# Optimization experiments

Hardware: AMD Instinct MI355X
Metric: run time of the kernel (lower is better)

## Reference

```python
import jax, jax.numpy as jnp
import numpy as np

BATCH = 64
N_NODES = 1000
SEQ = 12
FEAT = 4          # in_features_per_node // N_history
IN_CH = 48        # in_features_per_node, also GAT out_channels
HEADS = 2
OUT_FEAT = 2      # out_features_per_node
H1, H2 = 256, 128
N_TOTAL = BATCH * N_NODES
E = 1024000


def setup_inputs() -> dict:
    key = jax.random.key(0)
    ks = jax.random.split(key, 16)
    s = 0.05
    return {
        "x": jax.random.normal(ks[0], (N_TOTAL, IN_CH), jnp.float32),
        "edge_index": jax.random.randint(ks[1], (2, E), 0, N_TOTAL, jnp.int64),
        "W_gat": jax.random.normal(ks[2], (IN_CH, HEADS * IN_CH), jnp.float32) * s,
        "att_src": jax.random.normal(ks[3], (HEADS, IN_CH), jnp.float32) * s,
        "att_dst": jax.random.normal(ks[4], (HEADS, IN_CH), jnp.float32) * s,
        "gat_bias": jax.random.normal(ks[5], (IN_CH,), jnp.float32) * s,
        "W_ih1": jax.random.normal(ks[6], (4 * H1, N_NODES * FEAT), jnp.float32) * s,
        "W_hh1": jax.random.normal(ks[7], (4 * H1, H1), jnp.float32) * s,
        "b1": jnp.zeros((4 * H1,), jnp.float32),
        "W_ih2": jax.random.normal(ks[8], (4 * H2, H1), jnp.float32) * s,
        "W_hh2": jax.random.normal(ks[9], (4 * H2, H2), jnp.float32) * s,
        "b2": jnp.zeros((4 * H2,), jnp.float32),
        "W_out": jax.random.normal(ks[10], (N_NODES * OUT_FEAT, H2), jnp.float32) * s,
        "b_out": jnp.zeros((N_NODES * OUT_FEAT,), jnp.float32),
    }


def _gat_conv(x, edge_index, W_gat, att_src, att_dst, gat_bias):
    """PyG GATConv, heads=HEADS, concat=False (mean over heads), add_self_loops=True."""
    N = x.shape[0]
    h = (x @ W_gat).reshape(N, HEADS, IN_CH)              # [N,H,C]
    a_src = jnp.einsum('nhc,hc->nh', h, att_src)          # [N,H]
    a_dst = jnp.einsum('nhc,hc->nh', h, att_dst)
    loops = jnp.arange(N, dtype=edge_index.dtype)
    src = jnp.concatenate([edge_index[0], loops])         # [E+N]
    dst = jnp.concatenate([edge_index[1], loops])
    e = jax.nn.leaky_relu(a_src[src] + a_dst[dst], 0.2)   # [E+N,H]
    # segment-softmax over incoming edges of each destination node
    m = jnp.full((N, HEADS), -jnp.inf, e.dtype).at[dst].max(e)
    w = jnp.exp(e - m[dst])
    denom = jax.ops.segment_sum(w, dst, num_segments=N)
    alpha = w / (denom[dst] + 1e-16)                      # [E+N,H]
    msg = h[src] * alpha[:, :, None]                      # [E+N,H,C]
    out = jax.ops.segment_sum(msg, dst, num_segments=N)   # [N,H,C]
    return out.mean(axis=1) + gat_bias                    # [N,C]


def _lstm(x_seq, W_ih, W_hh, b):
    """Single-layer LSTM, PyTorch gate order (i,f,g,o). x_seq: [T,B,D]."""
    Hs = W_hh.shape[1]
    B = x_seq.shape[1]
    xw = jnp.einsum('tbd,gd->tbg', x_seq, W_ih) + b       # precompute input proj

    def step(carry, xt):
        h, c = carry
        g = xt + h @ W_hh.T
        i, f, gg, o = jnp.split(g, 4, axis=-1)
        i, f, o = jax.nn.sigmoid(i), jax.nn.sigmoid(f), jax.nn.sigmoid(o)
        c = f * c + i * jnp.tanh(gg)
        h = o * jnp.tanh(c)
        return (h, c), h

    h0 = jnp.zeros((B, Hs), x_seq.dtype)
    _, ys = jax.lax.scan(step, (h0, h0), xw)
    return ys                                             # [T,B,Hs]


def reference(x, edge_index, W_gat, att_src, att_dst, gat_bias,
              W_ih1, W_hh1, b1, W_ih2, W_hh2, b2, W_out, b_out):
    g = _gat_conv(x, edge_index, W_gat, att_src, att_dst, gat_bias)  # [N_total, 48]
    # (B, N_nodes, SEQ, FEAT) -> movedim(2,0) -> (SEQ, B, N_nodes*FEAT)
    g = g.reshape(BATCH, N_NODES, SEQ, FEAT)
    g = jnp.moveaxis(g, 2, 0).reshape(SEQ, BATCH, N_NODES * FEAT)
    y = _lstm(g, W_ih1, W_hh1, b1)
    y = _lstm(y, W_ih2, W_hh2, b2)
    last = y[-1]                                          # [B, H2]
    out = last @ W_out.T + b_out                          # [B, N_nodes*OUT_FEAT]
    return out.reshape(BATCH * N_NODES, OUT_FEAT)
```

## Files before the change

kernel.cpp:

```cpp
#include <hip/hip_runtime.h>
#include <hip/hip_fp16.h>
#include <math.h>

#define NTOT   64000
#define NNODE  1000
#define NBATCH 64
#define NSEQ   12
#define NE     1024000

typedef _Float16 half8 __attribute__((ext_vector_type(8)));
typedef float f32x4 __attribute__((ext_vector_type(4)));

__device__ __forceinline__ float lrelu(float x){ return x > 0.f ? x : 0.2f*x; }
__device__ __forceinline__ float sigmoidf_(float x){ return 1.f/(1.f+__expf(-x)); }

__global__ void __launch_bounds__(256) k_gat_count(const float* __restrict__ x, const float* __restrict__ Wg,
                       const float* __restrict__ att_s, const float* __restrict__ att_d,
                       __half* __restrict__ hfeat, float* __restrict__ asrc, float* __restrict__ adst,
                       const int* __restrict__ ei, int* __restrict__ cnt,
                       const float* __restrict__ Wih1, const float* __restrict__ Whh1,
                       const float* __restrict__ Wih2, const float* __restrict__ Whh2,
                       _Float16* __restrict__ Bh, __half* __restrict__ Wt){
  if (blockIdx.x >= 4250){
    int blk = blockIdx.x - 4250;
    if (blk < 4000){
      int i = blk*256 + threadIdx.x;
      float4 v = *(const float4*)(Wih1 + (size_t)i*4);
      union { _Float16 h[4]; uint2 u; } o;
      o.h[0] = (_Float16)v.x; o.h[1] = (_Float16)v.y;
      o.h[2] = (_Float16)v.z; o.h[3] = (_Float16)v.w;
      *(uint2*)(Bh + (size_t)i*4) = o.u;
      return;
    }
    int i = (blk-4000)*256 + threadIdx.x;
    if (i < 262144){ int q = i>>10, r = i&1023; Wt[i] = __float2half(Whh1[r*256+q]); return; }
    i -= 262144;
    if (i < 131072){ int q = i>>9, r = i&511; Wt[262144+i] = __float2half(Wih2[r*256+q]); return; }
    i -= 131072;
    if (i < 65536){ int q = i>>9, r = i&511; Wt[393216+i] = __float2half(Whh2[(size_t)r*128+q]); }
    return;
  }
  if (blockIdx.x >= 250){
    int e = (blockIdx.x - 250)*256 + threadIdx.x;
    if (e < NE) atomicAdd(&cnt[ei[NE + e]], 1);
    return;
  }
  __shared__ __align__(16) float Ws[48*96];
  __shared__ __align__(16) float as_s[96];
  __shared__ __align__(16) float ad_s[96];
  for (int i = threadIdx.x; i < 48*96; i += 256) Ws[i] = Wg[i];
  if (threadIdx.x < 96){ as_s[threadIdx.x] = att_s[threadIdx.x]; ad_s[threadIdx.x] = att_d[threadIdx.x]; }
  __syncthreads();
  int n = blockIdx.x * 256 + threadIdx.x;
  float xr[48];
  const float4* xv = (const float4*)(x + (size_t)n*48);
  #pragma unroll
  for (int q = 0; q < 12; ++q){ float4 v = xv[q]; xr[q*4]=v.x; xr[q*4+1]=v.y; xr[q*4+2]=v.z; xr[q*4+3]=v.w; }
  float a0=0.f,a1=0.f,d0=0.f,d1=0.f;
  __half* hrow = hfeat + (size_t)n*96;
  for (int j4 = 0; j4 < 96; j4 += 4){
    float ax=0.f, ay=0.f, az=0.f, aw=0.f;
    #pragma unroll 8
    for (int k = 0; k < 48; ++k){
      float4 wv = *(const float4*)&Ws[k*96 + j4];
      float xk = xr[k];
      ax += wv.x*xk; ay += wv.y*xk; az += wv.z*xk; aw += wv.w*xk;
    }
    __half2 p0; p0.x = __float2half(ax); p0.y = __float2half(ay);
    __half2 p1; p1.x = __float2half(az); p1.y = __float2half(aw);
    *(__half2*)(hrow + j4)     = p0;
    *(__half2*)(hrow + j4 + 2) = p1;
    float4 as4 = *(const float4*)&as_s[j4];
    float4 ad4 = *(const float4*)&ad_s[j4];
    float sdot = ax*as4.x + ay*as4.y + az*as4.z + aw*as4.w;
    float ddot = ax*ad4.x + ay*ad4.y + az*ad4.z + aw*ad4.w;
    if (j4 < 48){ a0 += sdot; d0 += ddot; }
    else        { a1 += sdot; d1 += ddot; }
  }
  asrc[n*2]=a0; asrc[n*2+1]=a1; adst[n*2]=d0; adst[n*2+1]=d1;
}

__global__ void __launch_bounds__(256) k_scan1(const int* __restrict__ cnt, int* __restrict__ wsum){
  int w = (blockIdx.x*256 + threadIdx.x) >> 6;
  int lane = threadIdx.x & 63;
  int v = cnt[w*64 + lane];
  int t = v;
  #pragma unroll
  for (int d = 1; d < 64; d <<= 1) t += __shfl_xor(t, d);
  if (lane == 0) wsum[w] = t;
}

__global__ void __launch_bounds__(1024) k_scan2(int* __restrict__ wsum){
  __shared__ int tmp[1024];
  int k = threadIdx.x;
  int v = (k < 1000) ? wsum[k] : 0;
  tmp[k] = v; __syncthreads();
  for (int d = 1; d < 1024; d <<= 1){
    int t = (k >= d) ? tmp[k-d] : 0;
    __syncthreads();
    tmp[k] += t;
    __syncthreads();
  }
  if (k < 1000) wsum[k] = tmp[k] - v;
}

__global__ void __launch_bounds__(256) k_scan3(const int* __restrict__ cnt, const int* __restrict__ wpre,
                                               int* __restrict__ offs, int* __restrict__ cursor){
  int w = (blockIdx.x*256 + threadIdx.x) >> 6;
  int lane = threadIdx.x & 63;
  int i = w*64 + lane;
  int v = cnt[i];
  int x = v;
  #pragma unroll
  for (int d = 1; d < 64; d <<= 1){
    int t = __shfl_up(x, d);
    if (lane >= d) x += t;
  }
  int excl = wpre[w] + x - v;
  offs[i] = excl; cursor[i] = excl;
  if (i == NTOT-1) offs[NTOT] = excl + v;
}

__global__ void k_scatter(const int* __restrict__ ei, int* __restrict__ cursor, int* __restrict__ csr){
  int e = blockIdx.x*256 + threadIdx.x;
  if (e < NE){
    int d = ei[NE + e], s = ei[e];
    int pos = atomicAdd(&cursor[d], 1);
    csr[pos] = s;
  }
}

__global__ void __launch_bounds__(256) k_node(const __half* __restrict__ hf, const float* __restrict__ asrc,
                      const float* __restrict__ adst, const int* __restrict__ offs,
                      const int* __restrict__ csr, const float* __restrict__ bias,
                      _Float16* __restrict__ xseqh){
  __shared__ float gsh[4][96];
  int wv = threadIdx.x >> 6, lane = threadIdx.x & 63;
  int n = blockIdx.x*4 + wv;
  int off = offs[n], deg = offs[n+1] - off;
  const float2* as2 = (const float2*)asrc;
  float2 adn = ((const float2*)adst)[n];
  float2 asn = as2[n];
  float es0 = __expf(lrelu(asn.x + adn.x));
  float es1 = __expf(lrelu(asn.y + adn.y));
  if (lane < 48){
    int cl = lane;
    bool h0 = (lane < 24);
    float wself = h0 ? es0 : es1;
    float ssum = wself;
    float2 acc;
    {
      __half2 r2 = *(const __half2*)(hf + (size_t)n*96 + 2*cl);
      float2 r = __half22float2(r2);
      acc.x = r.x*wself; acc.y = r.y*wself;
    }
    int i = 0;
    for (; i + 8 <= deg; i += 8){
      int ss[8];
      #pragma unroll
      for (int j = 0; j < 8; ++j) ss[j] = csr[off+i+j];
      float2 aa[8];
      #pragma unroll
      for (int j = 0; j < 8; ++j) aa[j] = as2[ss[j]];
      __half2 rr[8];
      #pragma unroll
      for (int j = 0; j < 8; ++j) rr[j] = *(const __half2*)(hf + (size_t)ss[j]*96 + 2*cl);
      #pragma unroll
      for (int j = 0; j < 8; ++j){
        float w0 = __expf(lrelu(aa[j].x + adn.x));
        float w1 = __expf(lrelu(aa[j].y + adn.y));
        float ws = h0 ? w0 : w1;
        float2 r = __half22float2(rr[j]);
        acc.x += r.x*ws; acc.y += r.y*ws;
        ssum += ws;
      }
    }
    for (; i + 4 <= deg; i += 4){
      int ss[4];
      #pragma unroll
      for (int j = 0; j < 4; ++j) ss[j] = csr[off+i+j];
      float2 aa[4];
      #pragma unroll
      for (int j = 0; j < 4; ++j) aa[j] = as2[ss[j]];
      __half2 rr[4];
      #pragma unroll
      for (int j = 0; j < 4; ++j) rr[j] = *(const __half2*)(hf + (size_t)ss[j]*96 + 2*cl);
      #pragma unroll
      for (int j = 0; j < 4; ++j){
        float w0 = __expf(lrelu(aa[j].x + adn.x));
        float w1 = __expf(lrelu(aa[j].y + adn.y));
        float ws = h0 ? w0 : w1;
        float2 r = __half22float2(rr[j]);
        acc.x += r.x*ws; acc.y += r.y*ws;
        ssum += ws;
      }
    }
    for (; i < deg; ++i){
      int s = csr[off+i];
      float2 a = as2[s];
      __half2 r2 = *(const __half2*)(hf + (size_t)s*96 + 2*cl);
      float w0 = __expf(lrelu(a.x + adn.x));
      float w1 = __expf(lrelu(a.y + adn.y));
      float ws = h0 ? w0 : w1;
      float2 r = __half22float2(r2);
      acc.x += r.x*ws; acc.y += r.y*ws;
      ssum += ws;
    }
    float inv = 1.f/(ssum + 1e-16f);
    gsh[wv][2*cl] = acc.x*inv; gsh[wv][2*cl+1] = acc.y*inv;
  }
  __syncthreads();
  if (lane < 48){
    float g = 0.5f*(gsh[wv][lane] + gsh[wv][48+lane]) + bias[lane];
    int b = n / 1000, node = n - b*1000;
    int t = lane >> 2, f = lane & 3;
    xseqh[((size_t)(t*64 + b))*4000 + node*4 + f] = (_Float16)g;
  }
}

__global__ void __launch_bounds__(256) k_gemm1h(const _Float16* __restrict__ A,
                        const _Float16* __restrict__ B, float* __restrict__ part){
  __shared__ _Float16 As[64*40];
  __shared__ _Float16 Bs[64*40];
  int tid = threadIdx.x;
  int w = tid >> 6, l = tid & 63;
  int m0 = blockIdx.x*64, n0 = blockIdx.y*64;
  int k0 = blockIdx.z*800;
  int fr = l & 15, fk = (l >> 4)*8;
  f32x4 acc0 = {0.f,0.f,0.f,0.f}, acc1 = acc0, acc2 = acc0, acc3 = acc0;
  int ra = tid >> 2, ca = (tid & 3)*8;
  const _Float16* Ap = A + (size_t)(m0+ra)*4000 + k0 + ca;
  const _Float16* Bp = B + (size_t)(n0+ra)*4000 + k0 + ca;
  _Float16* Asw = &As[ra*40 + ca];
  _Float16* Bsw = &Bs[ra*40 + ca];
  half8 pa = *(const half8*)Ap;
  half8 pb = *(const half8*)Bp;
  for (int kk = 0; kk < 800; kk += 32){
    *(half8*)Asw = pa;
    *(half8*)Bsw = pb;
    __syncthreads();
    if (kk + 32 < 800){
      pa = *(const half8*)(Ap + kk + 32);
      pb = *(const half8*)(Bp + kk + 32);
    }
    half8 af  = *(const half8*)&As[(w*16 + fr)*40 + fk];
    half8 bf0 = *(const half8*)&Bs[( 0 + fr)*40 + fk];
    half8 bf1 = *(const half8*)&Bs[(16 + fr)*40 + fk];
    half8 bf2 = *(const half8*)&Bs[(32 + fr)*40 + fk];
    half8 bf3 = *(const half8*)&Bs[(48 + fr)*40 + fk];
    acc0 = __builtin_amdgcn_mfma_f32_16x16x32_f16(af, bf0, acc0, 0, 0, 0);
    acc1 = __builtin_amdgcn_mfma_f32_16x16x32_f16(af, bf1, acc1, 0, 0, 0);
    acc2 = __builtin_amdgcn_mfma_f32_16x16x32_f16(af, bf2, acc2, 0, 0, 0);
    acc3 = __builtin_amdgcn_mfma_f32_16x16x32_f16(af, bf3, acc3, 0, 0, 0);
    __syncthreads();
  }
  int mrow = m0 + w*16 + (l >> 4)*4;
  int ncol = n0 + (l & 15);
  #pragma unroll
  for (int r = 0; r < 4; ++r){
    float* cp = part + ((size_t)blockIdx.z*768 + mrow + r)*1024 + ncol;
    cp[0]  = acc0[r];
    cp[16] = acc1[r];
    cp[32] = acc2[r];
    cp[48] = acc3[r];
  }
}

__device__ __forceinline__ void mac8(float* acc, uint4 wv, float hq){
  const __half2* hp = (const __half2*)&wv;
  float2 f0 = __half22float2(hp[0]);
  float2 f1 = __half22float2(hp[1]);
  float2 f2 = __half22float2(hp[2]);
  float2 f3 = __half22float2(hp[3]);
  acc[0] += f0.x*hq; acc[1] += f0.y*hq;
  acc[2] += f1.x*hq; acc[3] += f1.y*hq;
  acc[4] += f2.x*hq; acc[5] += f2.y*hq;
  acc[6] += f3.x*hq; acc[7] += f3.y*hq;
}

__global__ void __launch_bounds__(1024) k_lstm(
    const float* __restrict__ part, const float* __restrict__ b1,
    const __half* __restrict__ W1, const __half* __restrict__ W2i,
    const __half* __restrict__ W2h, const float* __restrict__ b2,
    float* __restrict__ h2o){
  __shared__ float h1s[256];
  __shared__ float h2s[128];
  __shared__ __align__(16) float pA[8192];
  __shared__ __align__(16) float pB[8192];
  int t = threadIdx.x;
  int b = blockIdx.x;
  int kk1 = t >> 7, c1c = (t & 127) * 8;
  int kk2 = t >> 6, c2c = (t & 63) * 8;
  int u2 = t - 256;
  float cc1 = 0.f, cc2 = 0.f;
  float b2r[4] = {0.f,0.f,0.f,0.f};
  if (t >= 256 && t < 384){
    #pragma unroll
    for (int gi = 0; gi < 4; ++gi) b2r[gi] = b2[gi*128 + u2];
  }
  float b1r[4] = {0.f,0.f,0.f,0.f};
  if (t < 256){
    #pragma unroll
    for (int gi = 0; gi < 4; ++gi) b1r[gi] = b1[gi*256 + t];
  }
  if (t < 256) h1s[t] = 0.f;
  if (t < 128) h2s[t] = 0.f;
  __syncthreads();

  for (int k = 0; k <= NSEQ; ++k){
    float xg[4] = {0.f,0.f,0.f,0.f};
    if (k < NSEQ && t < 256){
      const float* pr = part + ((size_t)k*64 + b)*1024 + t;
      #pragma unroll
      for (int gi = 0; gi < 4; ++gi){
        float s = b1r[gi];
        #pragma unroll
        for (int ss = 0; ss < 5; ++ss) s += pr[(size_t)ss*786432 + gi*256];
        xg[gi] = s;
      }
    }
    if (k < NSEQ){
      float acc[8] = {0,0,0,0,0,0,0,0};
      const __half* wp = W1 + (size_t)(kk1*32)*1024 + c1c;
      const float* hb = &h1s[kk1*32];
      #pragma unroll 4
      for (int q = 0; q < 32; ++q)
        mac8(acc, *(const uint4*)(wp + (size_t)q*1024), hb[q]);
      float4 w0; w0.x=acc[0]; w0.y=acc[1]; w0.z=acc[2]; w0.w=acc[3];
      float4 w1; w1.x=acc[4]; w1.y=acc[5]; w1.z=acc[6]; w1.w=acc[7];
      *(float4*)&pA[kk1*1024 + c1c]     = w0;
      *(float4*)&pA[kk1*1024 + c1c + 4] = w1;
    }
    if (k >= 1){
      float acch[8] = {0,0,0,0,0,0,0,0};
      const __half* wi = W2i + (size_t)(kk2*16)*512 + c2c;
      const float* hb1 = &h1s[kk2*16];
      #pragma unroll 4
      for (int q = 0; q < 16; ++q)
        mac8(acch, *(const uint4*)(wi + (size_t)q*512), hb1[q]);
      const __half* wh = W2h + (size_t)(kk2*8)*512 + c2c;
      const float* hb2 = &h2s[kk2*8];
      #pragma unroll 4
      for (int q = 0; q < 8; ++q)
        mac8(acch, *(const uint4*)(wh + (size_t)q*512), hb2[q]);
      float4 w0; w0.x=acch[0]; w0.y=acch[1]; w0.z=acch[2]; w0.w=acch[3];
      float4 w1; w1.x=acch[4]; w1.y=acch[5]; w1.z=acch[6]; w1.w=acch[7];
      *(float4*)&pB[kk2*512 + c2c]     = w0;
      *(float4*)&pB[kk2*512 + c2c + 4] = w1;
    }
    __syncthreads();
    if (k < NSEQ && t < 256){
      float g[4];
      #pragma unroll
      for (int gi = 0; gi < 4; ++gi){
        float s = xg[gi];
        #pragma unroll
        for (int kk = 0; kk < 8; ++kk) s += pA[kk*1024 + gi*256 + t];
        g[gi] = s;
      }
      float i_ = sigmoidf_(g[0]);
      float f_ = sigmoidf_(g[1]);
      float gg = tanhf(g[2]);
      float o_ = sigmoidf_(g[3]);
      cc1 = f_*cc1 + i_*gg;
      h1s[t] = o_*tanhf(cc1);
    }
    if (k >= 1 && t >= 256 && t < 384){
      float g[4];
      #pragma unroll
      for (int gi = 0; gi < 4; ++gi){
        float s = b2r[gi];
        #pragma unroll
        for (int kk = 0; kk < 16; ++kk) s += pB[kk*512 + gi*128 + u2];
        g[gi] = s;
      }
      float i_ = sigmoidf_(g[0]);
      float f_ = sigmoidf_(g[1]);
      float gg = tanhf(g[2]);
      float o_ = sigmoidf_(g[3]);
      cc2 = f_*cc2 + i_*gg;
      h2s[u2] = o_*tanhf(cc2);
    }
    __syncthreads();
  }
  if (t >= 256 && t < 384) h2o[(size_t)b*128 + u2] = h2s[u2];
}

__global__ void __launch_bounds__(256) k_out(const float* __restrict__ h2, const float* __restrict__ Wout,
                     const float* __restrict__ bout, float* __restrict__ out){
  __shared__ __align__(16) float hs[8][128];
  int t = threadIdx.x;
  int b0 = blockIdx.y * 8;
  #pragma unroll
  for (int r = 0; r < 4; ++r){
    int idx = r*256 + t;
    hs[idx >> 7][idx & 127] = h2[(size_t)(b0 + (idx >> 7))*128 + (idx & 127)];
  }
  __syncthreads();
  if (t >= 250) return;
  int j = blockIdx.x*250 + t;
  const float4* w = (const float4*)(Wout + (size_t)j*128);
  float bj = bout[j];
  float d[8];
  #pragma unroll
  for (int bb = 0; bb < 8; ++bb) d[bb] = bj;
  for (int q = 0; q < 32; ++q){
    float4 wv = w[q];
    #pragma unroll
    for (int bb = 0; bb < 8; ++bb){
      float4 hv = ((const float4*)hs[bb])[q];
      d[bb] += wv.x*hv.x + wv.y*hv.y + wv.z*hv.z + wv.w*hv.w;
    }
  }
  #pragma unroll
  for (int bb = 0; bb < 8; ++bb)
    out[(size_t)(b0+bb)*2000 + j] = d[bb];
}

extern "C" void kernel_launch(void* const* d_in, const int* in_sizes, int n_in,
                              void* d_out, int out_size, void* d_ws, size_t ws_size,
                              hipStream_t stream){
  const float* x     = (const float*)d_in[0];
  const int*   ei    = (const int*)d_in[1];
  const float* Wg    = (const float*)d_in[2];
  const float* att_s = (const float*)d_in[3];
  const float* att_d = (const float*)d_in[4];
  const float* gb    = (const float*)d_in[5];
  const float* Wih1  = (const float*)d_in[6];
  const float* Whh1  = (const float*)d_in[7];
  const float* b1    = (const float*)d_in[8];
  const float* Wih2  = (const float*)d_in[9];
  const float* Whh2  = (const float*)d_in[10];
  const float* b2    = (const float*)d_in[11];
  const float* Wout  = (const float*)d_in[12];
  const float* bout  = (const float*)d_in[13];
  float* out = (float*)d_out;

  char* w = (char*)d_ws;
  _Float16* xseqh = (_Float16*)w;
  float* part   = (float*)(w + 6291456);
  __half* hfeath = (__half*)(w + 12288000);
  _Float16* Bh  = (_Float16*)(w + 24576000);
  __half* W1h   = (__half*)(w + 32768000);
  float* h2o    = (float*)(w + 33685504);
  char*  p2 = w + 36864000;
  float* asrc   = (float*)(p2);
  float* adst   = (float*)(p2 + 512000);
  int*   cnt    = (int*)(p2 + 1024000);
  int*   offs   = (int*)(p2 + 1280000);
  int*   cursor = (int*)(p2 + 1536256);
  int*   csr    = (int*)(p2 + 1792256);
  int*   wsum   = csr;

  hipMemsetAsync(cnt, 0, NTOT*sizeof(int), stream);

  k_gat_count<<<10042, 256, 0, stream>>>(x, Wg, att_s, att_d, hfeath, asrc, adst, ei, cnt,
                                         Wih1, Whh1, Wih2, Whh2, Bh, W1h);
  k_scan1<<<250, 256, 0, stream>>>(cnt, wsum);
  k_scan2<<<1, 1024, 0, stream>>>(wsum);
  k_scan3<<<250, 256, 0, stream>>>(cnt, wsum, offs, cursor);
  k_scatter<<<4000, 256, 0, stream>>>(ei, cursor, csr);
  k_node<<<16000, 256, 0, stream>>>(hfeath, asrc, adst, offs, csr, gb, xseqh);

  k_gemm1h<<<dim3(12,16,5), 256, 0, stream>>>(xseqh, Bh, part);

  k_lstm<<<NBATCH, 1024, 0, stream>>>(part, b1, W1h, W1h + 262144, W1h + 393216, b2, h2o);
  k_out<<<dim3(8,8), 256, 0, stream>>>(h2o, Wout, bout, out);
}
```

Measured before the change: 353.5 us.

## Fuse output projection into LSTM, double-buffer GEMM smem, vectorize scatter

The output linear layer moves into the tail of the LSTM kernel. W_out is pre-transposed to fp16 during the weight-conversion blocks of the first kernel, which removes one kernel launch and the round trip of h2 through global memory. The fp16 input-projection GEMM now double-buffers its shared-memory tiles, so each k-step needs one barrier instead of two. The CSR scatter now handles two edges per thread with int2 loads. The trade-offs are extra conversion work in the first kernel, and an output GEMV of only 64 blocks inside the serial LSTM kernel, where it may be slow.

```diff
diff --git a/kernel.cpp b/kernel.cpp
--- a/kernel.cpp
+++ b/kernel.cpp
@@ -20,6 +20,7 @@
                        const int* __restrict__ ei, int* __restrict__ cnt,
                        const float* __restrict__ Wih1, const float* __restrict__ Whh1,
                        const float* __restrict__ Wih2, const float* __restrict__ Whh2,
+                       const float* __restrict__ Wout,
                        _Float16* __restrict__ Bh, __half* __restrict__ Wt){
   if (blockIdx.x >= 4250){
     int blk = blockIdx.x - 4250;
@@ -37,7 +38,9 @@
     i -= 262144;
     if (i < 131072){ int q = i>>9, r = i&511; Wt[262144+i] = __float2half(Wih2[r*256+q]); return; }
     i -= 131072;
-    if (i < 65536){ int q = i>>9, r = i&511; Wt[393216+i] = __float2half(Whh2[(size_t)r*128+q]); }
+    if (i < 65536){ int q = i>>9, r = i&511; Wt[393216+i] = __float2half(Whh2[(size_t)r*128+q]); return; }
+    i -= 65536;
+    if (i < 256000){ int q = i/2000, r = i - q*2000; Wt[458752+i] = __float2half(Wout[(size_t)r*128+q]); }
     return;
   }
   if (blockIdx.x >= 250){
@@ -122,11 +125,14 @@
 }
 
 __global__ void k_scatter(const int* __restrict__ ei, int* __restrict__ cursor, int* __restrict__ csr){
-  int e = blockIdx.x*256 + threadIdx.x;
-  if (e < NE){
-    int d = ei[NE + e], s = ei[e];
-    int pos = atomicAdd(&cursor[d], 1);
-    csr[pos] = s;
+  int e0 = (blockIdx.x*256 + threadIdx.x)*2;
+  if (e0 < NE){
+    int2 d2 = *(const int2*)(ei + NE + e0);
+    int2 s2 = *(const int2*)(ei + e0);
+    int p0 = atomicAdd(&cursor[d2.x], 1);
+    csr[p0] = s2.x;
+    int p1 = atomicAdd(&cursor[d2.y], 1);
+    csr[p1] = s2.y;
   }
 }
 
@@ -220,8 +226,8 @@
 
 __global__ void __launch_bounds__(256) k_gemm1h(const _Float16* __restrict__ A,
                         const _Float16* __restrict__ B, float* __restrict__ part){
-  __shared__ _Float16 As[64*40];
-  __shared__ _Float16 Bs[64*40];
+  __shared__ _Float16 As[2][64*40];
+  __shared__ _Float16 Bs[2][64*40];
   int tid = threadIdx.x;
   int w = tid >> 6, l = tid & 63;
   int m0 = blockIdx.x*64, n0 = blockIdx.y*64;
@@ -231,28 +237,34 @@
   int ra = tid >> 2, ca = (tid & 3)*8;
   const _Float16* Ap = A + (size_t)(m0+ra)*4000 + k0 + ca;
   const _Float16* Bp = B + (size_t)(n0+ra)*4000 + k0 + ca;
-  _Float16* Asw = &As[ra*40 + ca];
-  _Float16* Bsw = &Bs[ra*40 + ca];
+  int soff = ra*40 + ca;
   half8 pa = *(const half8*)Ap;
   half8 pb = *(const half8*)Bp;
+  *(half8*)&As[0][soff] = pa;
+  *(half8*)&Bs[0][soff] = pb;
+  __syncthreads();
+  int cur = 0;
   for (int kk = 0; kk < 800; kk += 32){
-    *(half8*)Asw = pa;
-    *(half8*)Bsw = pb;
-    __syncthreads();
-    if (kk + 32 < 800){
+    bool more = (kk + 32 < 800);
+    if (more){
       pa = *(const half8*)(Ap + kk + 32);
       pb = *(const half8*)(Bp + kk + 32);
     }
-    half8 af  = *(const half8*)&As[(w*16 + fr)*40 + fk];
-    half8 bf0 = *(const half8*)&Bs[( 0 + fr)*40 + fk];
-    half8 bf1 = *(const half8*)&Bs[(16 + fr)*40 + fk];
-    half8 bf2 = *(const half8*)&Bs[(32 + fr)*40 + fk];
-    half8 bf3 = *(const half8*)&Bs[(48 + fr)*40 + fk];
+    half8 af  = *(const half8*)&As[cur][(w*16 + fr)*40 + fk];
+    half8 bf0 = *(const half8*)&Bs[cur][( 0 + fr)*40 + fk];
+    half8 bf1 = *(const half8*)&Bs[cur][(16 + fr)*40 + fk];
+    half8 bf2 = *(const half8*)&Bs[cur][(32 + fr)*40 + fk];
+    half8 bf3 = *(const half8*)&Bs[cur][(48 + fr)*40 + fk];
     acc0 = __builtin_amdgcn_mfma_f32_16x16x32_f16(af, bf0, acc0, 0, 0, 0);
     acc1 = __builtin_amdgcn_mfma_f32_16x16x32_f16(af, bf1, acc1, 0, 0, 0);
     acc2 = __builtin_amdgcn_mfma_f32_16x16x32_f16(af, bf2, acc2, 0, 0, 0);
     acc3 = __builtin_amdgcn_mfma_f32_16x16x32_f16(af, bf3, acc3, 0, 0, 0);
+    if (more){
+      *(half8*)&As[cur^1][soff] = pa;
+      *(half8*)&Bs[cur^1][soff] = pb;
+    }
     __syncthreads();
+    cur ^= 1;
   }
   int mrow = m0 + w*16 + (l >> 4)*4;
   int ncol = n0 + (l & 15);
@@ -282,7 +294,8 @@
     const float* __restrict__ part, const float* __restrict__ b1,
     const __half* __restrict__ W1, const __half* __restrict__ W2i,
     const __half* __restrict__ W2h, const float* __restrict__ b2,
-    float* __restrict__ h2o){
+    const __half* __restrict__ Wt_o, const float* __restrict__ bout,
+    float* __restrict__ out){
   __shared__ float h1s[256];
   __shared__ float h2s[128];
   __shared__ __align__(16) float pA[8192];
@@ -383,38 +396,17 @@
     }
     __syncthreads();
   }
-  if (t >= 256 && t < 384) h2o[(size_t)b*128 + u2] = h2s[u2];
-}
-
-__global__ void __launch_bounds__(256) k_out(const float* __restrict__ h2, const float* __restrict__ Wout,
-                     const float* __restrict__ bout, float* __restrict__ out){
-  __shared__ __align__(16) float hs[8][128];
-  int t = threadIdx.x;
-  int b0 = blockIdx.y * 8;
   #pragma unroll
-  for (int r = 0; r < 4; ++r){
-    int idx = r*256 + t;
-    hs[idx >> 7][idx & 127] = h2[(size_t)(b0 + (idx >> 7))*128 + (idx & 127)];
-  }
-  __syncthreads();
-  if (t >= 250) return;
-  int j = blockIdx.x*250 + t;
-  const float4* w = (const float4*)(Wout + (size_t)j*128);
-  float bj = bout[j];
-  float d[8];
-  #pragma unroll
-  for (int bb = 0; bb < 8; ++bb) d[bb] = bj;
-  for (int q = 0; q < 32; ++q){
-    float4 wv = w[q];
-    #pragma unroll
-    for (int bb = 0; bb < 8; ++bb){
-      float4 hv = ((const float4*)hs[bb])[q];
-      d[bb] += wv.x*hv.x + wv.y*hv.y + wv.z*hv.z + wv.w*hv.w;
-    }
-  }
-  #pragma unroll
-  for (int bb = 0; bb < 8; ++bb)
-    out[(size_t)(b0+bb)*2000 + j] = d[bb];
+  for (int jj = 0; jj < 2; ++jj){
+    int j = t + jj*1024;
+    if (j < 2000){
+      float acc = bout[j];
+      #pragma unroll 8
+      for (int q = 0; q < 128; ++q)
+        acc += __half2float(Wt_o[(size_t)q*2000 + j]) * h2s[q];
+      out[(size_t)b*2000 + j] = acc;
+    }
+  }
 }
 
 extern "C" void kernel_launch(void* const* d_in, const int* in_sizes, int n_in,
@@ -442,7 +434,6 @@
   __half* hfeath = (__half*)(w + 12288000);
   _Float16* Bh  = (_Float16*)(w + 24576000);
   __half* W1h   = (__half*)(w + 32768000);
-  float* h2o    = (float*)(w + 33685504);
   char*  p2 = w + 36864000;
   float* asrc   = (float*)(p2);
   float* adst   = (float*)(p2 + 512000);
@@ -454,16 +445,16 @@
 
   hipMemsetAsync(cnt, 0, NTOT*sizeof(int), stream);
 
-  k_gat_count<<<10042, 256, 0, stream>>>(x, Wg, att_s, att_d, hfeath, asrc, adst, ei, cnt,
-                                         Wih1, Whh1, Wih2, Whh2, Bh, W1h);
+  k_gat_count<<<11042, 256, 0, stream>>>(x, Wg, att_s, att_d, hfeath, asrc, adst, ei, cnt,
+                                         Wih1, Whh1, Wih2, Whh2, Wout, Bh, W1h);
   k_scan1<<<250, 256, 0, stream>>>(cnt, wsum);
   k_scan2<<<1, 1024, 0, stream>>>(wsum);
   k_scan3<<<250, 256, 0, stream>>>(cnt, wsum, offs, cursor);
-  k_scatter<<<4000, 256, 0, stream>>>(ei, cursor, csr);
+  k_scatter<<<2000, 256, 0, stream>>>(ei, cursor, csr);
   k_node<<<16000, 256, 0, stream>>>(hfeath, asrc, adst, offs, csr, gb, xseqh);
 
   k_gemm1h<<<dim3(12,16,5), 256, 0, stream>>>(xseqh, Bh, part);
 
-  k_lstm<<<NBATCH, 1024, 0, stream>>>(part, b1, W1h, W1h + 262144, W1h + 393216, b2, h2o);
-  k_out<<<dim3(8,8), 256, 0, stream>>>(h2o, Wout, bout, out);
-}
+  k_lstm<<<NBATCH, 1024, 0, stream>>>(part, b1, W1h, W1h + 262144, W1h + 393216, b2,
+                                      W1h + 458752, bout, out);
+}
```

Measured after the change: 355.9 us (median of 2 runs). No clear change (+0.7%).
